# Kernel tuning notes

Hardware: AMD Instinct MI355X
Metric: run time of the kernel (lower is better)

Reference implementation:

```python
import jax, jax.numpy as jnp
import numpy as np
import math

B, T, E, H = 4, 1024, 1024, 16
D = E // H  # head_dim = 64
EPS = 1e-5


def setup_inputs() -> dict:
    key = jax.random.key(0)
    k1, k2, k3 = jax.random.split(key, 3)
    x = jax.random.normal(k1, (B, T, E), dtype=jnp.float32)
    scale = jnp.ones((E,), dtype=jnp.float32)
    w_qkv = jax.random.normal(k2, (3 * E, E), dtype=jnp.float32) * (1.0 / math.sqrt(E))
    w_proj = jax.random.normal(k3, (E, E), dtype=jnp.float32) * (1.0 / math.sqrt(E))
    return {"x": x, "scale": scale, "w_qkv": w_qkv, "w_proj": w_proj}


def reference(x, scale, w_qkv, w_proj):
    # RMSNorm
    xn = x * jax.lax.rsqrt(jnp.mean(x * x, axis=-1, keepdims=True) + EPS) * scale
    # QKV projection (torch Linear: y = x @ W.T)
    qkv = jnp.einsum('bte,fe->btf', xn, w_qkv)  # [B,T,3E]
    q, k, v = jnp.split(qkv, 3, axis=-1)
    # [B,T,E] -> [B,H,T,D]
    q = q.reshape(B, T, H, D).transpose(0, 2, 1, 3)
    k = k.reshape(B, T, H, D).transpose(0, 2, 1, 3)
    v = v.reshape(B, T, H, D).transpose(0, 2, 1, 3)
    # causal attention
    attn = jnp.einsum('bhqd,bhkd->bhqk', q, k) / math.sqrt(D)
    causal = jnp.tril(jnp.ones((T, T), dtype=bool))
    attn = jnp.where(causal, attn, -jnp.inf)
    attn = jax.nn.softmax(attn, axis=-1)
    out = jnp.einsum('bhqk,bhkd->bhqd', attn, v)  # [B,H,T,D]
    out = out.transpose(0, 2, 1, 3).reshape(B, T, E)
    # output projection
    return jnp.einsum('bte,fe->btf', out, w_proj)
```

## Files before the change

kernel.cpp:

```cpp
#include <hip/hip_runtime.h>
#include <hip/hip_bf16.h>
#include <stdint.h>

#define B_SZ 4
#define T_SEQ 1024
#define E_DIM 1024
#define NH 16
#define HD 64
#define THREE_E 3072
#define NTOK 4096

typedef unsigned short u16;
typedef unsigned int u32;
using short8v = __attribute__((ext_vector_type(8))) short;
using short4v = __attribute__((ext_vector_type(4))) short;
using f32x4 = __attribute__((ext_vector_type(4))) float;

__device__ __forceinline__ u16 f2bf(float f) {
    union { float f; uint32_t u; } c; c.f = f;
    uint32_t u = c.u;
    uint32_t r = (u + 0x7FFFu + ((u >> 16) & 1u)) >> 16;
    return (u16)r;
}

__device__ __forceinline__ u32 cvt_pk_bf16(float lo, float hi) {
    u32 r;
    asm("v_cvt_pk_bf16_f32 %0, %1, %2" : "=v"(r) : "v"(lo), "v"(hi));
    return r;
}

__device__ __forceinline__ void gload_lds16(const u16* g, u16* l) {
    __builtin_amdgcn_global_load_lds((const __attribute__((address_space(1))) void*)g,
                                     (__attribute__((address_space(3))) void*)l, 16, 0, 0);
}

__global__ __launch_bounds__(256) void prep_kernel(const float* __restrict__ x,
                                                   const float* __restrict__ scale,
                                                   const float* __restrict__ wq,
                                                   const float* __restrict__ wp,
                                                   u16* __restrict__ xn,
                                                   u16* __restrict__ wqb,
                                                   u16* __restrict__ wpb) {
    int bx = blockIdx.x;
    int tid = threadIdx.x;
    if (bx < 4096) {
        int row = bx;
        const float4* xr = reinterpret_cast<const float4*>(x + (size_t)row * E_DIM);
        float4 v = xr[tid];
        float ss = v.x * v.x + v.y * v.y + v.z * v.z + v.w * v.w;
        for (int off = 32; off > 0; off >>= 1) ss += __shfl_xor(ss, off);
        __shared__ float red[4];
        if ((tid & 63) == 0) red[tid >> 6] = ss;
        __syncthreads();
        float total = red[0] + red[1] + red[2] + red[3];
        float rs = rsqrtf(total * (1.0f / E_DIM) + 1e-5f);
        float4 s = reinterpret_cast<const float4*>(scale)[tid];
        u16* o = xn + (size_t)row * E_DIM + tid * 4;
        o[0] = f2bf(v.x * rs * s.x);
        o[1] = f2bf(v.y * rs * s.y);
        o[2] = f2bf(v.z * rs * s.z);
        o[3] = f2bf(v.w * rs * s.w);
    } else {
        const int NQ = (THREE_E * E_DIM) / 4;
        const int NP = (E_DIM * E_DIM) / 4;
        int i = (bx - 4096) * 256 + tid;
        if (i < NQ) {
            float4 v = reinterpret_cast<const float4*>(wq)[i];
            u16* o = wqb + (size_t)i * 4;
            o[0] = f2bf(v.x); o[1] = f2bf(v.y); o[2] = f2bf(v.z); o[3] = f2bf(v.w);
        } else if (i < NQ + NP) {
            int j = i - NQ;
            float4 v = reinterpret_cast<const float4*>(wp)[j];
            u16* o = wpb + (size_t)j * 4;
            o[0] = f2bf(v.x); o[1] = f2bf(v.y); o[2] = f2bf(v.z); o[3] = f2bf(v.w);
        }
    }
}

template <int BN, bool OUT_BF16>
__global__ __launch_bounds__(256) void gemm_lds_kernel(const u16* __restrict__ A,
                                                       const u16* __restrict__ Bw,
                                                       void* __restrict__ C,
                                                       int N, int K) {
    constexpr int NFR = BN / 32;
    __shared__ u16 As[128 * 64];
    __shared__ u16 Bs[BN * 64];
    int tid = threadIdx.x;
    int lane = tid & 63, wid = tid >> 6;
    int lq = lane & 15, lg = lane >> 4;

    int gx = gridDim.x;
    int nwg = gx * gridDim.y;
    int orig = blockIdx.y * gx + blockIdx.x;
    int cpx = nwg >> 3;
    int swz = (orig & 7) * cpx + (orig >> 3);
    int bx = swz % gx, by = swz / gx;
    int mblk = by * 128, nblk = bx * BN;

    int srowA = wid * 32 + (lane >> 3);
    int srowB = wid * (BN / 4) + (lane >> 3);
    int csw = ((lane & 7) ^ ((lane >> 3) & 7)) * 8;
    const u16* gA = A + (size_t)(mblk + srowA) * K + csw;
    const u16* gB = Bw + (size_t)(nblk + srowB) * K + csw;
    u16* lA = As + wid * 2048;
    u16* lB = Bs + wid * (BN / 4) * 64;

    f32x4 acc[4][NFR] = {};
    int m0w = (wid >> 1) * 64;
    int n0w = (wid & 1) * (BN / 2);
    int r7 = lq & 7;
    const int NT = K / 64;

#pragma unroll
    for (int i = 0; i < 4; ++i) gload_lds16(gA + (size_t)i * 8 * K, lA + i * 512);
#pragma unroll
    for (int i = 0; i < NFR; ++i) gload_lds16(gB + (size_t)i * 8 * K, lB + i * 512);

    for (int t = 0; t < NT; ++t) {
        __syncthreads();
        short8v af[2][4], bf[2][NFR];
#pragma unroll
        for (int kk = 0; kk < 2; ++kk) {
#pragma unroll
            for (int mi = 0; mi < 4; ++mi)
                af[kk][mi] = *reinterpret_cast<const short8v*>(
                    &As[(m0w + mi * 16 + lq) * 64 + ((kk * 4 + lg) ^ r7) * 8]);
#pragma unroll
            for (int ni = 0; ni < NFR; ++ni)
                bf[kk][ni] = *reinterpret_cast<const short8v*>(
                    &Bs[(n0w + ni * 16 + lq) * 64 + ((kk * 4 + lg) ^ r7) * 8]);
        }
        __builtin_amdgcn_s_setprio(1);
#pragma unroll
        for (int mi = 0; mi < 4; ++mi)
#pragma unroll
            for (int ni = 0; ni < NFR; ++ni)
                acc[mi][ni] = __builtin_amdgcn_mfma_f32_16x16x32_bf16(af[0][mi], bf[0][ni], acc[mi][ni], 0, 0, 0);
        __builtin_amdgcn_s_setprio(0);
        __syncthreads();
        if (t + 1 < NT) {
            int k0 = (t + 1) * 64;
#pragma unroll
            for (int i = 0; i < 4; ++i) gload_lds16(gA + k0 + (size_t)i * 8 * K, lA + i * 512);
#pragma unroll
            for (int i = 0; i < NFR; ++i) gload_lds16(gB + k0 + (size_t)i * 8 * K, lB + i * 512);
        }
        __builtin_amdgcn_sched_barrier(0);
        __builtin_amdgcn_s_setprio(1);
#pragma unroll
        for (int mi = 0; mi < 4; ++mi)
#pragma unroll
            for (int ni = 0; ni < NFR; ++ni)
                acc[mi][ni] = __builtin_amdgcn_mfma_f32_16x16x32_bf16(af[1][mi], bf[1][ni], acc[mi][ni], 0, 0, 0);
        __builtin_amdgcn_s_setprio(0);
    }
#pragma unroll
    for (int mi = 0; mi < 4; ++mi) {
#pragma unroll
        for (int ni = 0; ni < NFR; ++ni) {
#pragma unroll
            for (int j = 0; j < 4; ++j) {
                int row = mblk + m0w + mi * 16 + lg * 4 + j;
                int col = nblk + n0w + ni * 16 + lq;
                float val = acc[mi][ni][j];
                if (OUT_BF16)
                    ((u16*)C)[(size_t)row * N + col] = f2bf(val);
                else
                    ((float*)C)[(size_t)row * N + col] = val;
            }
        }
    }
}

template <bool DIAG>
__device__ __forceinline__ void attn_tile(const u16 (*__restrict__ Kt)[72],
                                          const u16 (*__restrict__ Vt)[72],
                                          const short8v* __restrict__ qf,
                                          f32x4* __restrict__ o,
                                          float& l_r,
                                          int lq, int lg, int w4, int kt64, int qg) {
    const float CLOG = 0.18033688011112042f;
    const float MOFF = 11.541560327111707f;
    int ksmax = DIAG ? w4 : 3;
    f32x4 st[4] = {};
    __builtin_amdgcn_s_setprio(1);
#pragma unroll
    for (int ks = 0; ks < 4; ++ks) {
        if (ks <= ksmax) {
            short8v a0 = *reinterpret_cast<const short8v*>(&Kt[ks * 16 + lq][lg * 8]);
            short8v a1 = *reinterpret_cast<const short8v*>(&Kt[ks * 16 + lq][32 + lg * 8]);
            st[ks] = __builtin_amdgcn_mfma_f32_16x16x32_bf16(a0, qf[0], st[ks], 0, 0, 0);
            st[ks] = __builtin_amdgcn_mfma_f32_16x16x32_bf16(a1, qf[1], st[ks], 0, 0, 0);
        }
    }
    __builtin_amdgcn_s_setprio(0);
    float p[4][4];
    float psum = 0.f;
#pragma unroll
    for (int ks = 0; ks < 4; ++ks)
#pragma unroll
        for (int j = 0; j < 4; ++j) {
            float v = st[ks][j];
            if (DIAG) {
                int kg = kt64 + ks * 16 + lg * 4 + j;
                v = (ks <= ksmax && kg <= qg) ? v : -INFINITY;
            }
            float pv = exp2f(fmaf(v, CLOG, -MOFF));
            p[ks][j] = pv;
            psum += pv;
        }
    l_r += psum;
    union { u32 w2[2]; short4v v; } pa[4];
#pragma unroll
    for (int ks = 0; ks < 4; ++ks) {
        pa[ks].w2[0] = cvt_pk_bf16(p[ks][0], p[ks][1]);
        pa[ks].w2[1] = cvt_pk_bf16(p[ks][2], p[ks][3]);
    }
    __builtin_amdgcn_s_setprio(1);
#pragma unroll
    for (int ni = 0; ni < 4; ++ni) {
        int d = ni * 16 + lq;
        int sw = ((d >> 3) & 7) << 3;
        const u16* vrow = Vt[d];
#pragma unroll
        for (int ks = 0; ks < 4; ++ks) {
            if (ks <= ksmax) {
                short4v vb = *reinterpret_cast<const short4v*>(&vrow[(ks * 16 + lg * 4) ^ sw]);
                o[ni] = __builtin_amdgcn_mfma_f32_16x16x16bf16_1k(pa[ks].v, vb, o[ni], 0, 0, 0);
            }
        }
    }
    __builtin_amdgcn_s_setprio(0);
}

__global__ __launch_bounds__(512) void attn_kernel(const u16* __restrict__ qkv,
                                                   u16* __restrict__ out) {
    int tid = threadIdx.x;
    int lane = tid & 63, wid = tid >> 6;
    int lq = lane & 15, lg = lane >> 4;
    int w4 = wid & 3;
    bool is_hi = wid >= 4;
    int bh = blockIdx.y;
    int b = bh >> 4, h = bh & 15;
    int qlo_blk = blockIdx.x;
    int qhi_blk = 15 - qlo_blk;
    int myblk = is_hi ? qhi_blk : qlo_blk;
    int qt = myblk * 64 + w4 * 16;

    const u16* base = qkv + (size_t)b * T_SEQ * THREE_E;
    const u16* Qb = base + h * HD;
    const u16* Kb = base + E_DIM + h * HD;

    __shared__ __align__(16) u16 Kt[2][64][72];
    __shared__ __align__(16) u16 Vt[2][64][72];

    short8v qf[2];
    {
        const u16* qr = Qb + (size_t)(qt + lq) * THREE_E + lg * 8;
        qf[0] = *reinterpret_cast<const short8v*>(qr);
        qf[1] = *reinterpret_cast<const short8v*>(qr + 32);
    }
    f32x4 o[4] = {};
    float l_r = 0.f;
    int qg = qt + lq;

    int row_s = tid >> 3, c8 = tid & 7;
    short8v kreg, vreg;

    {
        const u16* src = Kb + (size_t)row_s * THREE_E + c8 * 8;
        kreg = *reinterpret_cast<const short8v*>(src);
        vreg = *reinterpret_cast<const short8v*>(src + E_DIM);
    }
    {
        *reinterpret_cast<short8v*>(&Kt[0][row_s][c8 * 8]) = kreg;
        int rs = row_s ^ (c8 << 3);
#pragma unroll
        for (int e = 0; e < 8; ++e) Vt[0][c8 * 8 + e][rs] = (u16)vreg[e];
    }
    if (qhi_blk >= 1) {
        const u16* src = Kb + (size_t)(64 + row_s) * THREE_E + c8 * 8;
        kreg = *reinterpret_cast<const short8v*>(src);
        vreg = *reinterpret_cast<const short8v*>(src + E_DIM);
    }
    __syncthreads();

    for (int kt = 0; kt <= qhi_blk; ++kt) {
        int cur = kt & 1;
        if (kt < qhi_blk) {
            *reinterpret_cast<short8v*>(&Kt[cur ^ 1][row_s][c8 * 8]) = kreg;
            int rs = row_s ^ (c8 << 3);
#pragma unroll
            for (int e = 0; e < 8; ++e) Vt[cur ^ 1][c8 * 8 + e][rs] = (u16)vreg[e];
            if (kt + 1 < qhi_blk) {
                const u16* src = Kb + (size_t)((kt + 2) * 64 + row_s) * THREE_E + c8 * 8;
                kreg = *reinterpret_cast<const short8v*>(src);
                vreg = *reinterpret_cast<const short8v*>(src + E_DIM);
            }
        }
        if (is_hi) {
            if (kt < qhi_blk)
                attn_tile<false>(Kt[cur], Vt[cur], qf, o, l_r, lq, lg, w4, kt * 64, qg);
            else
                attn_tile<true>(Kt[cur], Vt[cur], qf, o, l_r, lq, lg, w4, kt * 64, qg);
        } else {
            if (kt < qlo_blk)
                attn_tile<false>(Kt[cur], Vt[cur], qf, o, l_r, lq, lg, w4, kt * 64, qg);
            else if (kt == qlo_blk)
                attn_tile<true>(Kt[cur], Vt[cur], qf, o, l_r, lq, lg, w4, kt * 64, qg);
        }
        __syncthreads();
    }
    float lf = l_r;
    lf += __shfl_xor(lf, 16); lf += __shfl_xor(lf, 32);
#pragma unroll
    for (int j = 0; j < 4; ++j) {
        float linv = 1.0f / __shfl(lf, lg * 4 + j);
        size_t row = (size_t)b * T_SEQ + qt + lg * 4 + j;
#pragma unroll
        for (int ni = 0; ni < 4; ++ni)
            out[row * E_DIM + h * HD + ni * 16 + lq] = f2bf(o[ni][j] * linv);
    }
}

extern "C" void kernel_launch(void* const* d_in, const int* in_sizes, int n_in,
                              void* d_out, int out_size, void* d_ws, size_t ws_size,
                              hipStream_t stream) {
    const float* x = (const float*)d_in[0];
    const float* scale = (const float*)d_in[1];
    const float* w_qkv = (const float*)d_in[2];
    const float* w_proj = (const float*)d_in[3];
    float* out = (float*)d_out;

    char* ws = (char*)d_ws;
    u16* xn   = (u16*)(ws);
    u16* wqb  = (u16*)(ws + (8ull << 20));
    u16* wpb  = (u16*)(ws + (14ull << 20));
    u16* qkv  = (u16*)(ws + (16ull << 20));
    u16* aout = (u16*)(ws + (40ull << 20));

    prep_kernel<<<dim3(8192), dim3(256), 0, stream>>>(x, scale, w_qkv, w_proj, xn, wqb, wpb);
    gemm_lds_kernel<128, true><<<dim3(THREE_E / 128, NTOK / 128), dim3(256), 0, stream>>>(
        xn, wqb, (void*)qkv, THREE_E, E_DIM);
    attn_kernel<<<dim3(8, B_SZ * NH), dim3(512), 0, stream>>>(qkv, aout);
    gemm_lds_kernel<64, false><<<dim3(E_DIM / 64, NTOK / 128), dim3(256), 0, stream>>>(
        aout, wpb, (void*)out, E_DIM, E_DIM);
}
```

Measured before the change: 89.51 us.

## Add double-buffered 256x192 QKV GEMM with 8 waves and interleaved LDS reads

Replaces the QKV projection GEMM with a new kernel using 256x192 tiles, 512 threads, and double-buffered LDS. Global loads for tile t+2 are issued while MFMAs run on the current buffer, and LDS fragment reads are split into phases separated by barriers. The aim is to hide memory latency and raise MFMA utilization for the largest GEMM. It also moves the first-half MFMAs in the output-projection GEMM to after the prefetch issue, which lengthens register lifetimes. The large LDS footprint (about 112 KB per block) limits occupancy.

```diff
diff --git a/kernel.cpp b/kernel.cpp
--- a/kernel.cpp
+++ b/kernel.cpp
@@ -77,6 +77,131 @@
     }
 }
 
+#define MF12(RA, RB, MO)                                                        \
+    do {                                                                        \
+        _Pragma("unroll") for (int mi_ = 0; mi_ < 4; ++mi_)                     \
+            _Pragma("unroll") for (int ni_ = 0; ni_ < 3; ++ni_)                 \
+                acc[(MO) + mi_][ni_] = __builtin_amdgcn_mfma_f32_16x16x32_bf16( \
+                    (RA)[mi_], (RB)[ni_], acc[(MO) + mi_][ni_], 0, 0, 0);       \
+    } while (0)
+
+template <int K>
+__global__ __launch_bounds__(512, 2) void gemm_qkv_kernel(const u16* __restrict__ A,
+                                                          const u16* __restrict__ Bw,
+                                                          u16* __restrict__ C, int N) {
+    constexpr int NT = K / 64;
+    __shared__ u16 As[2][256 * 64];
+    __shared__ u16 Bs[2][192 * 64];
+    int tid = threadIdx.x;
+    int lane = tid & 63, wid = tid >> 6;
+    int lq = lane & 15, lg = lane >> 4;
+    int wm = wid >> 2, wn = wid & 3;
+
+    int gx = gridDim.x;
+    int nwg = gx * gridDim.y;
+    int orig = blockIdx.y * gx + blockIdx.x;
+    int cpx = nwg >> 3;
+    int swz = (orig & 7) * cpx + (orig >> 3);
+    int bx = swz % gx, by = swz / gx;
+    int mblk = by * 256, nblk = bx * 192;
+
+    int srw = wid * 8 + (lane >> 3);
+    int csw = ((lane & 7) ^ ((lane >> 3) & 7)) * 8;
+    const u16* gA = A + (size_t)(mblk + srw) * K + csw;
+    const u16* gB = Bw + (size_t)(nblk + srw) * K + csw;
+    int ldsw = wid * 512;
+
+    auto STAGE = [&](int t) {
+        int buf = t & 1;
+        int k0 = t * 64;
+#pragma unroll
+        for (int s = 0; s < 4; ++s)
+            gload_lds16(gA + (size_t)s * 64 * K + k0, &As[buf][s * 4096 + ldsw]);
+#pragma unroll
+        for (int s = 0; s < 3; ++s)
+            gload_lds16(gB + (size_t)s * 64 * K + k0, &Bs[buf][s * 4096 + ldsw]);
+    };
+
+    int r7 = lq & 7;
+    int aoff = (wm * 128 + lq) * 64;
+    int boff = (wn * 48 + lq) * 64;
+    int c0 = ((0 + lg) ^ r7) * 8;
+    int c1 = ((4 + lg) ^ r7) * 8;
+
+    f32x4 acc[8][3] = {};
+
+    STAGE(0);
+    STAGE(1);
+    asm volatile("s_waitcnt vmcnt(7)" ::: "memory");
+    __builtin_amdgcn_s_barrier();
+
+    for (int t = 0; t < NT; ++t) {
+        int buf = t & 1;
+        const u16* Ab = As[buf];
+        const u16* Bb = Bs[buf];
+        short8v ra0[4], ra1[4], ra2[4], ra3[4], rb0[3], rb1[3];
+#pragma unroll
+        for (int mi = 0; mi < 4; ++mi) {
+            ra0[mi] = *reinterpret_cast<const short8v*>(Ab + aoff + mi * 1024 + c0);
+            ra1[mi] = *reinterpret_cast<const short8v*>(Ab + aoff + (mi + 4) * 1024 + c0);
+        }
+#pragma unroll
+        for (int ni = 0; ni < 3; ++ni)
+            rb0[ni] = *reinterpret_cast<const short8v*>(Bb + boff + ni * 1024 + c0);
+        __builtin_amdgcn_s_barrier();
+        asm volatile("s_waitcnt lgkmcnt(0)" ::: "memory");
+        __builtin_amdgcn_sched_barrier(0);
+        __builtin_amdgcn_s_setprio(1);
+        MF12(ra0, rb0, 0);
+        __builtin_amdgcn_s_setprio(0);
+        __builtin_amdgcn_s_barrier();
+#pragma unroll
+        for (int mi = 0; mi < 4; ++mi)
+            ra2[mi] = *reinterpret_cast<const short8v*>(Ab + aoff + mi * 1024 + c1);
+        __builtin_amdgcn_s_barrier();
+        asm volatile("s_waitcnt lgkmcnt(0)" ::: "memory");
+        __builtin_amdgcn_sched_barrier(0);
+        __builtin_amdgcn_s_setprio(1);
+        MF12(ra1, rb0, 4);
+        __builtin_amdgcn_s_setprio(0);
+        __builtin_amdgcn_s_barrier();
+#pragma unroll
+        for (int mi = 0; mi < 4; ++mi)
+            ra3[mi] = *reinterpret_cast<const short8v*>(Ab + aoff + (mi + 4) * 1024 + c1);
+#pragma unroll
+        for (int ni = 0; ni < 3; ++ni)
+            rb1[ni] = *reinterpret_cast<const short8v*>(Bb + boff + ni * 1024 + c1);
+        __builtin_amdgcn_s_barrier();
+        asm volatile("s_waitcnt lgkmcnt(0)" ::: "memory");
+        __builtin_amdgcn_sched_barrier(0);
+        __builtin_amdgcn_s_setprio(1);
+        MF12(ra2, rb1, 0);
+        __builtin_amdgcn_s_setprio(0);
+        __builtin_amdgcn_s_barrier();
+        if (t + 2 < NT) {
+            STAGE(t + 2);
+            asm volatile("s_waitcnt vmcnt(7)" ::: "memory");
+        } else {
+            asm volatile("s_waitcnt vmcnt(0)" ::: "memory");
+        }
+        __builtin_amdgcn_sched_barrier(0);
+        __builtin_amdgcn_s_setprio(1);
+        MF12(ra3, rb1, 4);
+        __builtin_amdgcn_s_setprio(0);
+        __builtin_amdgcn_s_barrier();
+    }
+#pragma unroll
+    for (int mi = 0; mi < 8; ++mi)
+#pragma unroll
+        for (int ni = 0; ni < 3; ++ni)
+#pragma unroll
+            for (int j = 0; j < 4; ++j) {
+                int row = mblk + wm * 128 + mi * 16 + lg * 4 + j;
+                int col = nblk + wn * 48 + ni * 16 + lq;
+                C[(size_t)row * N + col] = f2bf(acc[mi][ni][j]);
+            }
+}
+
 template <int BN, bool OUT_BF16>
 __global__ __launch_bounds__(256) void gemm_lds_kernel(const u16* __restrict__ A,
                                                        const u16* __restrict__ Bw,
@@ -130,13 +255,6 @@
                 bf[kk][ni] = *reinterpret_cast<const short8v*>(
                     &Bs[(n0w + ni * 16 + lq) * 64 + ((kk * 4 + lg) ^ r7) * 8]);
         }
-        __builtin_amdgcn_s_setprio(1);
-#pragma unroll
-        for (int mi = 0; mi < 4; ++mi)
-#pragma unroll
-            for (int ni = 0; ni < NFR; ++ni)
-                acc[mi][ni] = __builtin_amdgcn_mfma_f32_16x16x32_bf16(af[0][mi], bf[0][ni], acc[mi][ni], 0, 0, 0);
-        __builtin_amdgcn_s_setprio(0);
         __syncthreads();
         if (t + 1 < NT) {
             int k0 = (t + 1) * 64;
@@ -150,8 +268,10 @@
 #pragma unroll
         for (int mi = 0; mi < 4; ++mi)
 #pragma unroll
-            for (int ni = 0; ni < NFR; ++ni)
+            for (int ni = 0; ni < NFR; ++ni) {
+                acc[mi][ni] = __builtin_amdgcn_mfma_f32_16x16x32_bf16(af[0][mi], bf[0][ni], acc[mi][ni], 0, 0, 0);
                 acc[mi][ni] = __builtin_amdgcn_mfma_f32_16x16x32_bf16(af[1][mi], bf[1][ni], acc[mi][ni], 0, 0, 0);
+            }
         __builtin_amdgcn_s_setprio(0);
     }
 #pragma unroll
@@ -340,8 +460,8 @@
     u16* aout = (u16*)(ws + (40ull << 20));
 
     prep_kernel<<<dim3(8192), dim3(256), 0, stream>>>(x, scale, w_qkv, w_proj, xn, wqb, wpb);
-    gemm_lds_kernel<128, true><<<dim3(THREE_E / 128, NTOK / 128), dim3(256), 0, stream>>>(
-        xn, wqb, (void*)qkv, THREE_E, E_DIM);
+    gemm_qkv_kernel<E_DIM><<<dim3(THREE_E / 192, NTOK / 256), dim3(512), 0, stream>>>(
+        xn, wqb, qkv, THREE_E);
     attn_kernel<<<dim3(8, B_SZ * NH), dim3(512), 0, stream>>>(qkv, aout);
     gemm_lds_kernel<64, false><<<dim3(E_DIM / 64, NTOK / 128), dim3(256), 0, stream>>>(
         aout, wpb, (void*)out, E_DIM, E_DIM);
```

Measured after the change: 92.90 us. +3.8%, slower.
